# Optimization experiments

Hardware: AMD Instinct MI355X
Metric: run time of the kernel (lower is better)

## Reference

```python
import jax, jax.numpy as jnp
import numpy as np

N, D, D_A, D_B, R = 512, 4096, 256, 256, 4
B = 2048
U_END = D_B * R            # 1024
V_END = U_END + R * D_A    # 2048
B_END = V_END + D_B        # 2304
LN_EPS = 1e-5


def setup_inputs() -> dict:
    key = jax.random.key(0)
    k1, k2, k3, k4 = jax.random.split(key, 4)
    return {
        "h_A": jax.random.normal(k1, (B, D_A), dtype=jnp.float32),
        "pool_vectors": jax.random.normal(k2, (N, D), dtype=jnp.float32) * 0.02,
        "alpha": jax.random.uniform(k3, (B, N), dtype=jnp.float32),
        "W_base": jax.random.normal(k4, (D_B, D_A), dtype=jnp.float32) * 0.01,
        "b_base": jnp.zeros((D_B,), dtype=jnp.float32),
        "gamma": jnp.array(0.01, dtype=jnp.float32),
        "ln_scale": jnp.ones((D_A,), dtype=jnp.float32),
        "ln_bias": jnp.zeros((D_A,), dtype=jnp.float32),
    }


def reference(h_A, pool_vectors, alpha, W_base, b_base, gamma, ln_scale, ln_bias):
    # --- assemble ---
    U = pool_vectors[:, :U_END].reshape(N, D_B, R)          # [N, d_B, r]
    V = pool_vectors[:, U_END:V_END].reshape(N, R, D_A)     # [N, r, d_A]
    bias = pool_vectors[:, V_END:B_END]                     # [N, d_B]
    UV = jnp.einsum('ndr,nre->nde', U, V)                   # [N, d_B, d_A]
    W_assembled = W_base[None] + jnp.einsum('bn,nde->bde', alpha, UV)  # [B, d_B, d_A]
    b_assembled = b_base[None] + jnp.einsum('bn,nd->bd', alpha, bias)  # [B, d_B]
    # --- apply + residual + LayerNorm ---
    h_t = jnp.einsum('ba,bca->bc', h_A, W_assembled) + b_assembled     # [B, d_B]
    y = h_A + gamma * h_t
    mu = jnp.mean(y, axis=-1, keepdims=True)
    var = jnp.var(y, axis=-1, keepdims=True)
    y_norm = (y - mu) * jax.lax.rsqrt(var + LN_EPS)
    return y_norm * ln_scale + ln_bias
```

## Files before the change

### kernel.cpp

```cpp
#include <hip/hip_runtime.h>
#include <hip/hip_bf16.h>


typedef __attribute__((ext_vector_type(8))) short bf16x8;
typedef __attribute__((ext_vector_type(4))) float f32x4;
typedef unsigned short ushort_t;

#define LDA_X 2816
#define N_POOL 512
#define D_POOL 4096

__device__ __forceinline__ void gld16(const ushort_t* g, ushort_t* l) {
    __builtin_amdgcn_global_load_lds((__attribute__((address_space(1))) void*)g,
                                     (__attribute__((address_space(3))) void*)l, 16, 0, 0);
}

__device__ __forceinline__ ushort_t bfb(float x) {
    union { __hip_bfloat16 h; ushort_t u; } c; c.h = __float2bfloat16(x); return c.u;
}

__device__ __forceinline__ float bf2f(ushort_t u) {
    union { unsigned int i; float f; } c; c.i = ((unsigned int)u) << 16; return c.f;
}

__device__ __forceinline__ void write4(ushort_t* p, float4 v) {
    ushort4 w = {bfb(v.x), bfb(v.y), bfb(v.z), bfb(v.w)};
    *(ushort4*)p = w;
}

__global__ __launch_bounds__(256) void kFront(const float* __restrict__ hA,
                                              const float* __restrict__ pool,
                                              const float* __restrict__ alpha,
                                              const float* __restrict__ Wb,
                                              ushort_t* __restrict__ Xu,
                                              ushort_t* __restrict__ Mt,
                                              ushort_t* __restrict__ part) {
    __shared__ __align__(16) ushort_t shmem[16384];
    ushort_t* As = shmem;
    ushort_t* Bs = shmem + 8192;
    const int t = threadIdx.x;
    const int bid = blockIdx.x;

    if (bid >= 1024 && bid < 1536) {
        int idx = (bid - 1024) * 256 + t, c = idx >> 9, n = idx & 511;
        write4(Mt + (size_t)c * LDA_X + (n << 2), *(const float4*)&pool[(size_t)n * D_POOL + (c << 2)]);
        return;
    }

    const int w = t >> 6, l = t & 63, l16 = l & 15, l4 = l >> 4;
    const int wr = w >> 1, wc = w & 1;
    const int row = t >> 2, cs = t & 3;

    f32x4 acc[2][2];
    #pragma unroll
    for (int i = 0; i < 2; ++i)
        #pragma unroll
        for (int j = 0; j < 2; ++j) acc[i][j] = (f32x4){0.f, 0.f, 0.f, 0.f};

    float4 aR[4], bR[4];

    auto writeLDS_AB = [&](int buf) {
        #pragma unroll
        for (int p = 0; p < 4; ++p) {
            int c0 = (cs + p * 4) << 2;
            int off = row * 64 + (((c0 >> 3) ^ (row & 7)) << 3) + ((c0 >> 2) & 1) * 4;
            ushort4 ua = {bfb(aR[p].x), bfb(aR[p].y), bfb(aR[p].z), bfb(aR[p].w)};
            ushort4 ub = {bfb(bR[p].x), bfb(bR[p].y), bfb(bR[p].z), bfb(bR[p].w)};
            *(ushort4*)&As[buf * 4096 + off] = ua;
            *(ushort4*)&Bs[buf * 4096 + off] = ub;
        }
    };
    auto compute = [&](int buf) {
        bf16x8 af[2][2], bv[2][2];
        #pragma unroll
        for (int mi = 0; mi < 2; ++mi) {
            int arow = wr * 32 + mi * 16 + l16;
            #pragma unroll
            for (int ks = 0; ks < 2; ++ks)
                af[mi][ks] = *(const bf16x8*)&As[buf * 4096 + arow * 64 + (((ks * 4 + l4) ^ (arow & 7)) << 3)];
        }
        #pragma unroll
        for (int ni = 0; ni < 2; ++ni) {
            int brow = wc * 32 + ni * 16 + l16;
            #pragma unroll
            for (int ks = 0; ks < 2; ++ks)
                bv[ni][ks] = *(const bf16x8*)&Bs[buf * 4096 + brow * 64 + (((ks * 4 + l4) ^ (brow & 7)) << 3)];
        }
        #pragma unroll
        for (int ks = 0; ks < 2; ++ks)
            #pragma unroll
            for (int mi = 0; mi < 2; ++mi)
                #pragma unroll
                for (int ni = 0; ni < 2; ++ni)
                    acc[mi][ni] = __builtin_amdgcn_mfma_f32_16x16x32_bf16(af[mi][ks], bv[ni][ks], acc[mi][ni], 0, 0, 0);
    };
    auto epilogueLDS = [&]() {
        __syncthreads();
        float* sc = (float*)shmem;
        #pragma unroll
        for (int mi = 0; mi < 2; ++mi)
            #pragma unroll
            for (int ni = 0; ni < 2; ++ni)
                #pragma unroll
                for (int e = 0; e < 4; ++e)
                    sc[(wr * 32 + mi * 16 + l4 * 4 + e) * 64 + wc * 32 + ni * 16 + l16] = acc[mi][ni][e];
        __syncthreads();
    };

    if (bid < 1024) {
        const int bm0 = (bid >> 5) * 64, bn0 = (bid & 31) * 64;
        const int kk = bn0 + row;
        const float* bbase = pool + (size_t)(kk >> 2) * D_POOL + 1024 + (kk & 3) * 256;
        const float* abase = hA + (size_t)(bm0 + row) * 256;
        auto loadRegs = [&](int step) {
            const int a0 = step * 64;
            #pragma unroll
            for (int p = 0; p < 4; ++p) {
                int c0 = (cs + p * 4) << 2;
                aR[p] = *(const float4*)(abase + a0 + c0);
                bR[p] = *(const float4*)(bbase + a0 + c0);
            }
        };
        loadRegs(0); writeLDS_AB(0); __syncthreads();
        int cur = 0;
        #pragma unroll
        for (int it = 0; it < 3; ++it) {
            loadRegs(it + 1);
            compute(cur);
            writeLDS_AB(cur ^ 1);
            __syncthreads();
            cur ^= 1;
        }
        compute(cur);
        epilogueLDS();
        float* sc = (float*)shmem;
        const int r2 = t >> 2, c0 = (t & 3) * 16;
        const float* arow = alpha + (size_t)(bm0 + r2) * N_POOL;
        __align__(16) ushort_t u[16];
        #pragma unroll
        for (int j = 0; j < 16; ++j)
            u[j] = bfb(sc[r2 * 64 + c0 + j] * arow[(bn0 + c0 + j) >> 2]);
        ushort_t* dst = Xu + (size_t)(bm0 + r2) * LDA_X + bn0 + c0;
        *(uint4*)dst = ((uint4*)u)[0];
        *(uint4*)(dst + 8) = ((uint4*)u)[1];
        return;
    }

    if (bid < 1664) {
        const int b2 = bid - 1536;
        const int bm0 = (b2 >> 2) * 64, bc0 = (b2 & 3) * 64;
        const float* abase = hA + (size_t)(bm0 + row) * 256;
        const float* bbase = Wb + (size_t)(bc0 + row) * 256;
        auto loadRegs = [&](int step) {
            const int a0 = step * 64;
            #pragma unroll
            for (int p = 0; p < 4; ++p) {
                int c0 = (cs + p * 4) << 2;
                aR[p] = *(const float4*)(abase + a0 + c0);
                bR[p] = *(const float4*)(bbase + a0 + c0);
            }
        };
        loadRegs(0); writeLDS_AB(0); __syncthreads();
        int cur = 0;
        #pragma unroll
        for (int it = 0; it < 3; ++it) {
            loadRegs(it + 1);
            compute(cur);
            writeLDS_AB(cur ^ 1);
            __syncthreads();
            cur ^= 1;
        }
        compute(cur);
        epilogueLDS();
        float* sc = (float*)shmem;
        const int r2 = t >> 2, c0 = (t & 3) * 16;
        __align__(16) ushort_t u[16];
        #pragma unroll
        for (int j = 0; j < 16; ++j) u[j] = bfb(sc[r2 * 64 + c0 + j]);
        ushort_t* P = part + (size_t)8 * (2048 * 256) + (size_t)(bm0 + r2) * 256 + bc0 + c0;
        *(uint4*)P = ((uint4*)u)[0];
        *(uint4*)(P + 8) = ((uint4*)u)[1];
        return;
    }

    {
        const int b2 = bid - 1664;
        const int bm0 = (b2 >> 2) * 64, bc0 = (b2 & 3) * 64;
        const float* abase = alpha + (size_t)(bm0 + row) * N_POOL;
        const int cg = t & 63;
        const int jg = t >> 6;
        float bRv[16];
        auto loadRegsB = [&](int step) {
            const int j0 = step * 64;
            #pragma unroll
            for (int p = 0; p < 4; ++p) {
                int c0 = (cs + p * 4) << 2;
                aR[p] = *(const float4*)(abase + j0 + c0);
            }
            #pragma unroll
            for (int p = 0; p < 16; ++p)
                bRv[p] = pool[(size_t)(j0 + jg * 16 + p) * D_POOL + 2048 + bc0 + cg];
        };
        auto writeLDSB = [&](int buf) {
            #pragma unroll
            for (int p = 0; p < 4; ++p) {
                int c0 = (cs + p * 4) << 2;
                int off = row * 64 + (((c0 >> 3) ^ (row & 7)) << 3) + ((c0 >> 2) & 1) * 4;
                ushort4 ua = {bfb(aR[p].x), bfb(aR[p].y), bfb(aR[p].z), bfb(aR[p].w)};
                *(ushort4*)&As[buf * 4096 + off] = ua;
            }
            #pragma unroll
            for (int p = 0; p < 16; ++p) {
                int jj = jg * 16 + p;
                Bs[buf * 4096 + cg * 64 + (((jj >> 3) ^ (cg & 7)) << 3) + (jj & 7)] = bfb(bRv[p]);
            }
        };
        loadRegsB(0); writeLDSB(0); __syncthreads();
        int cur = 0;
        #pragma unroll
        for (int it = 0; it < 7; ++it) {
            loadRegsB(it + 1);
            compute(cur);
            writeLDSB(cur ^ 1);
            __syncthreads();
            cur ^= 1;
        }
        compute(cur);
        epilogueLDS();
        float* sc = (float*)shmem;
        const int r2 = t >> 2, c0 = (t & 3) * 16;
        __align__(16) ushort_t u[16];
        #pragma unroll
        for (int j = 0; j < 16; ++j) u[j] = bfb(sc[r2 * 64 + c0 + j]);
        ushort_t* P = part + (size_t)9 * (2048 * 256) + (size_t)(bm0 + r2) * 256 + bc0 + c0;
        *(uint4*)P = ((uint4*)u)[0];
        *(uint4*)(P + 8) = ((uint4*)u)[1];
    }
}

__global__ __launch_bounds__(256) void kB(const ushort_t* __restrict__ Xu,
                                          const ushort_t* __restrict__ Mt,
                                          ushort_t* __restrict__ part) {
    __shared__ __align__(16) ushort_t As[2][4096];
    __shared__ __align__(16) ushort_t Bs[2][4096];
    const int t = threadIdx.x;
    const int w = t >> 6, l = t & 63, l16 = l & 15, l4 = l >> 4;
    const int wr = w >> 1, wc = w & 1;
    const int bid = blockIdx.x;
    const int z = bid & 7;
    const int n = (bid >> 3) & 3;
    const int m = bid >> 5;
    const int bm0 = m * 64, bn0 = n * 64;
    const int kc0 = z * 256;
    const int srow = t >> 3;
    const int schunk = (t & 7) ^ (srow & 7);

    f32x4 acc[2][2];
    #pragma unroll
    for (int i = 0; i < 2; ++i)
        #pragma unroll
        for (int j = 0; j < 2; ++j) acc[i][j] = (f32x4){0.f, 0.f, 0.f, 0.f};

    auto stage = [&](int buf, int k0) {
        #pragma unroll
        for (int h = 0; h < 2; ++h) {
            gld16(Xu + (size_t)(bm0 + srow + h * 32) * LDA_X + k0 + schunk * 8,
                  &As[buf][h * 2048 + w * 512]);
            gld16(Mt + (size_t)(bn0 + srow + h * 32) * LDA_X + k0 + schunk * 8,
                  &Bs[buf][h * 2048 + w * 512]);
        }
    };
    auto compute = [&](int buf) {
        bf16x8 af[2][2], bv[2][2];
        #pragma unroll
        for (int mi = 0; mi < 2; ++mi) {
            int arow = wr * 32 + mi * 16 + l16;
            #pragma unroll
            for (int ks = 0; ks < 2; ++ks)
                af[mi][ks] = *(const bf16x8*)&As[buf][arow * 64 + (((ks * 4 + l4) ^ (arow & 7)) << 3)];
        }
        #pragma unroll
        for (int ni = 0; ni < 2; ++ni) {
            int brow = wc * 32 + ni * 16 + l16;
            #pragma unroll
            for (int ks = 0; ks < 2; ++ks)
                bv[ni][ks] = *(const bf16x8*)&Bs[buf][brow * 64 + (((ks * 4 + l4) ^ (brow & 7)) << 3)];
        }
        #pragma unroll
        for (int ks = 0; ks < 2; ++ks)
            #pragma unroll
            for (int mi = 0; mi < 2; ++mi)
                #pragma unroll
                for (int ni = 0; ni < 2; ++ni)
                    acc[mi][ni] = __builtin_amdgcn_mfma_f32_16x16x32_bf16(af[mi][ks], bv[ni][ks], acc[mi][ni], 0, 0, 0);
    };

    stage(0, kc0);
    __syncthreads();
    int cur = 0;
    #pragma unroll
    for (int it = 0; it < 3; ++it) {
        stage(cur ^ 1, kc0 + (it + 1) * 64);
        compute(cur);
        __syncthreads();
        cur ^= 1;
    }
    compute(cur);

    __syncthreads();
    float* sc = (float*)&As[0][0];
    #pragma unroll
    for (int mi = 0; mi < 2; ++mi)
        #pragma unroll
        for (int ni = 0; ni < 2; ++ni)
            #pragma unroll
            for (int e = 0; e < 4; ++e)
                sc[(wr * 32 + mi * 16 + l4 * 4 + e) * 64 + wc * 32 + ni * 16 + l16] = acc[mi][ni][e];
    __syncthreads();
    const int r2 = t >> 2, c0 = (t & 3) * 16;
    __align__(16) ushort_t u[16];
    #pragma unroll
    for (int j = 0; j < 16; ++j) u[j] = bfb(sc[r2 * 64 + c0 + j]);
    ushort_t* P = part + (size_t)z * (2048 * 256) + (size_t)(bm0 + r2) * 256 + bn0 + c0;
    *(uint4*)P = ((uint4*)u)[0];
    *(uint4*)(P + 8) = ((uint4*)u)[1];
}

__global__ __launch_bounds__(256) void kC(const ushort_t* __restrict__ part,
                                          const float* __restrict__ hA,
                                          const float* __restrict__ bb,
                                          const float* __restrict__ gamma_p,
                                          const float* __restrict__ lns,
                                          const float* __restrict__ lnb,
                                          float* __restrict__ out) {
    const int wave = threadIdx.x >> 6;
    const int lane = threadIdx.x & 63;
    const int b = blockIdx.x * 4 + wave;
    const float g = gamma_p[0];
    const size_t base = (size_t)b * 256 + lane * 4;

    float p0 = 0.f, p1 = 0.f, p2 = 0.f, p3 = 0.f;
    #pragma unroll
    for (int z = 0; z < 10; ++z) {
        ushort4 q = *(const ushort4*)&part[(size_t)z * 2048 * 256 + base];
        p0 += bf2f(q.x); p1 += bf2f(q.y); p2 += bf2f(q.z); p3 += bf2f(q.w);
    }
    float4 h  = *(const float4*)&hA[base];
    float4 b4 = *(const float4*)&bb[lane * 4];
    float y0 = h.x + g * (p0 + b4.x);
    float y1 = h.y + g * (p1 + b4.y);
    float y2 = h.z + g * (p2 + b4.z);
    float y3 = h.w + g * (p3 + b4.w);

    float sum = y0 + y1 + y2 + y3;
    float ss  = y0*y0 + y1*y1 + y2*y2 + y3*y3;
    #pragma unroll
    for (int off = 1; off < 64; off <<= 1) {
        sum += __shfl_xor(sum, off);
        ss  += __shfl_xor(ss, off);
    }
    float mu  = sum * (1.0f / 256.0f);
    float var = ss * (1.0f / 256.0f) - mu * mu;
    float inv = rsqrtf(var + 1e-5f);

    float4 sc = *(const float4*)&lns[lane * 4];
    float4 bi = *(const float4*)&lnb[lane * 4];
    float4 o;
    o.x = (y0 - mu) * inv * sc.x + bi.x;
    o.y = (y1 - mu) * inv * sc.y + bi.y;
    o.z = (y2 - mu) * inv * sc.z + bi.z;
    o.w = (y3 - mu) * inv * sc.w + bi.w;
    *(float4*)&out[base] = o;
}

extern "C" void kernel_launch(void* const* d_in, const int* in_sizes, int n_in,
                              void* d_out, int out_size, void* d_ws, size_t ws_size,
                              hipStream_t stream) {
    const float* hA    = (const float*)d_in[0];
    const float* pool  = (const float*)d_in[1];
    const float* alpha = (const float*)d_in[2];
    const float* Wb    = (const float*)d_in[3];
    const float* bb    = (const float*)d_in[4];
    const float* gamma = (const float*)d_in[5];
    const float* lns   = (const float*)d_in[6];
    const float* lnb   = (const float*)d_in[7];
    float* out = (float*)d_out;

    ushort_t* Xu   = (ushort_t*)d_ws;
    ushort_t* Mt   = Xu + (size_t)2048 * LDA_X;
    ushort_t* part = Mt + (size_t)256 * LDA_X;

    kFront<<<1792, 256, 0, stream>>>(hA, pool, alpha, Wb, Xu, Mt, part);
    kB<<<1024, 256, 0, stream>>>(Xu, Mt, part);
    kC<<<512, 256, 0, stream>>>(part, hA, bb, gamma, lns, lnb, out);
}
```

Baseline: 35.39 us.

## Fuse V-projection and U-expansion GEMMs into one kernel, keeping intermediate in LDS

Merges the front kernel's hA·V GEMM and the second-stage GEMM against U into a single kernel. Each block owns 64 batch rows and a 64-pool-vector slice, and keeps the alpha-scaled intermediate in LDS as bf16. This drops the global Xu/Mt workspaces, the transpose pass and one kernel launch. Per-block work grows (64x256 tiles, 512 blocks total), so occupancy is lower and fewer blocks are available to fill the GPU.

```diff
diff --git a/kernel.cpp b/kernel.cpp
--- a/kernel.cpp
+++ b/kernel.cpp
@@ -6,14 +6,8 @@
 typedef __attribute__((ext_vector_type(4))) float f32x4;
 typedef unsigned short ushort_t;
 
-#define LDA_X 2816
 #define N_POOL 512
 #define D_POOL 4096
-
-__device__ __forceinline__ void gld16(const ushort_t* g, ushort_t* l) {
-    __builtin_amdgcn_global_load_lds((__attribute__((address_space(1))) void*)g,
-                                     (__attribute__((address_space(3))) void*)l, 16, 0, 0);
-}
 
 __device__ __forceinline__ ushort_t bfb(float x) {
     union { __hip_bfloat16 h; ushort_t u; } c; c.h = __float2bfloat16(x); return c.u;
@@ -23,31 +17,192 @@
     union { unsigned int i; float f; } c; c.i = ((unsigned int)u) << 16; return c.f;
 }
 
-__device__ __forceinline__ void write4(ushort_t* p, float4 v) {
-    ushort4 w = {bfb(v.x), bfb(v.y), bfb(v.z), bfb(v.w)};
-    *(ushort4*)p = w;
-}
-
-__global__ __launch_bounds__(256) void kFront(const float* __restrict__ hA,
+__global__ __launch_bounds__(256) void kFused(const float* __restrict__ hA,
                                               const float* __restrict__ pool,
                                               const float* __restrict__ alpha,
                                               const float* __restrict__ Wb,
-                                              ushort_t* __restrict__ Xu,
-                                              ushort_t* __restrict__ Mt,
                                               ushort_t* __restrict__ part) {
-    __shared__ __align__(16) ushort_t shmem[16384];
-    ushort_t* As = shmem;
-    ushort_t* Bs = shmem + 8192;
+    __shared__ __align__(16) ushort_t shm[36864];
     const int t = threadIdx.x;
     const int bid = blockIdx.x;
-
-    if (bid >= 1024 && bid < 1536) {
-        int idx = (bid - 1024) * 256 + t, c = idx >> 9, n = idx & 511;
-        write4(Mt + (size_t)c * LDA_X + (n << 2), *(const float4*)&pool[(size_t)n * D_POOL + (c << 2)]);
+    const int w = t >> 6, l = t & 63, l16 = l & 15, l4 = l >> 4;
+
+    if (bid < 256) {
+        ushort_t* As = shm;
+        ushort_t* Bs = shm + 4096;
+        ushort_t* S_ = shm + 20480;
+        const int m = bid >> 3, z = bid & 7;
+        const int b0 = m * 64;
+
+        f32x4 acc[4][4];
+        #pragma unroll
+        for (int i = 0; i < 4; ++i)
+            #pragma unroll
+            for (int j = 0; j < 4; ++j) acc[i][j] = (f32x4){0.f, 0.f, 0.f, 0.f};
+
+        float4 regA[2], regB[8];
+        const int rA = t >> 2, cA = t & 3;
+
+        auto compute = [&](int buf) {
+            bf16x8 af[4], bv[4];
+            #pragma unroll
+            for (int mi = 0; mi < 4; ++mi) {
+                int ar = mi * 16 + l16;
+                af[mi] = *(const bf16x8*)&As[buf * 2048 + ar * 32 + ((l4 ^ ((ar >> 1) & 3)) << 3)];
+            }
+            #pragma unroll
+            for (int ni = 0; ni < 4; ++ni) {
+                int br = w * 64 + ni * 16 + l16;
+                bv[ni] = *(const bf16x8*)&Bs[buf * 8192 + br * 32 + ((l4 ^ ((br >> 1) & 3)) << 3)];
+            }
+            #pragma unroll
+            for (int mi = 0; mi < 4; ++mi)
+                #pragma unroll
+                for (int ni = 0; ni < 4; ++ni)
+                    acc[mi][ni] = __builtin_amdgcn_mfma_f32_16x16x32_bf16(af[mi], bv[ni], acc[mi][ni], 0, 0, 0);
+        };
+
+        const float* aBase = hA + (size_t)(b0 + rA) * 256;
+        auto loadA1 = [&](int st) {
+            regA[0] = *(const float4*)(aBase + st * 32 + cA * 8);
+            regA[1] = *(const float4*)(aBase + st * 32 + cA * 8 + 4);
+        };
+        auto loadB1 = [&](int st) {
+            #pragma unroll
+            for (int p = 0; p < 8; ++p) {
+                int n_off = w * 16 + p * 2 + (l >> 5);
+                int q = (l >> 3) & 3, a_off = (l & 7) * 4;
+                regB[p] = *(const float4*)&pool[(size_t)(z * 64 + n_off) * D_POOL + 1024 + q * 256 + st * 32 + a_off];
+            }
+        };
+        auto writeA = [&](int buf) {
+            int ch = cA ^ ((rA >> 1) & 3);
+            ushort4 u0 = {bfb(regA[0].x), bfb(regA[0].y), bfb(regA[0].z), bfb(regA[0].w)};
+            ushort4 u1 = {bfb(regA[1].x), bfb(regA[1].y), bfb(regA[1].z), bfb(regA[1].w)};
+            *(ushort4*)&As[buf * 2048 + rA * 32 + (ch << 3)] = u0;
+            *(ushort4*)&As[buf * 2048 + rA * 32 + (ch << 3) + 4] = u1;
+        };
+        auto writeB1 = [&](int buf) {
+            #pragma unroll
+            for (int p = 0; p < 8; ++p) {
+                int n_off = w * 16 + p * 2 + (l >> 5);
+                int q = (l >> 3) & 3;
+                int krel = n_off * 4 + q;
+                int chunk = (l & 7) >> 1, half = (l & 7) & 1;
+                ushort4 u = {bfb(regB[p].x), bfb(regB[p].y), bfb(regB[p].z), bfb(regB[p].w)};
+                *(ushort4*)&Bs[buf * 8192 + krel * 32 + ((chunk ^ ((krel >> 1) & 3)) << 3) + half * 4] = u;
+            }
+        };
+
+        loadA1(0); loadB1(0); writeA(0); writeB1(0);
+        __syncthreads();
+        int cur = 0;
+        #pragma unroll
+        for (int it = 0; it < 7; ++it) {
+            loadA1(it + 1); loadB1(it + 1);
+            compute(cur);
+            writeA(cur ^ 1); writeB1(cur ^ 1);
+            __syncthreads();
+            cur ^= 1;
+        }
+        compute(cur);
+
+        #pragma unroll
+        for (int mi = 0; mi < 4; ++mi)
+            #pragma unroll
+            for (int ni = 0; ni < 4; ++ni) {
+                int col = w * 64 + ni * 16 + l16;
+                #pragma unroll
+                for (int e = 0; e < 4; ++e) {
+                    int row = mi * 16 + l4 * 4 + e;
+                    float av = alpha[(size_t)(b0 + row) * N_POOL + z * 64 + (col >> 2)];
+                    int ch = (col >> 3) ^ (row & 7);
+                    S_[row * 256 + (ch << 3) + (col & 7)] = bfb(acc[mi][ni][e] * av);
+                }
+                acc[mi][ni] = (f32x4){0.f, 0.f, 0.f, 0.f};
+            }
+        __syncthreads();
+
+        auto loadB2 = [&](int st) {
+            #pragma unroll
+            for (int p = 0; p < 8; ++p) {
+                int n_off = w * 2 + (p >> 2);
+                int cblk = p & 3;
+                regB[p] = *(const float4*)&pool[(size_t)(z * 64 + st * 8 + n_off) * D_POOL + (cblk * 64 + l) * 4];
+            }
+        };
+        auto writeB2 = [&](int buf) {
+            #pragma unroll
+            for (int p = 0; p < 8; ++p) {
+                int n_off = w * 2 + (p >> 2);
+                int c = (p & 3) * 64 + l;
+                int chunk = n_off >> 1, half = n_off & 1;
+                ushort4 u = {bfb(regB[p].x), bfb(regB[p].y), bfb(regB[p].z), bfb(regB[p].w)};
+                *(ushort4*)&Bs[buf * 8192 + c * 32 + ((chunk ^ ((c >> 1) & 3)) << 3) + half * 4] = u;
+            }
+        };
+        auto compute2 = [&](int buf, int st) {
+            bf16x8 af[4], bv[4];
+            #pragma unroll
+            for (int mi = 0; mi < 4; ++mi) {
+                int ar = mi * 16 + l16;
+                int ch = (st * 4 + l4) ^ (ar & 7);
+                af[mi] = *(const bf16x8*)&S_[ar * 256 + (ch << 3)];
+            }
+            #pragma unroll
+            for (int ni = 0; ni < 4; ++ni) {
+                int br = w * 64 + ni * 16 + l16;
+                bv[ni] = *(const bf16x8*)&Bs[buf * 8192 + br * 32 + ((l4 ^ ((br >> 1) & 3)) << 3)];
+            }
+            #pragma unroll
+            for (int mi = 0; mi < 4; ++mi)
+                #pragma unroll
+                for (int ni = 0; ni < 4; ++ni)
+                    acc[mi][ni] = __builtin_amdgcn_mfma_f32_16x16x32_bf16(af[mi], bv[ni], acc[mi][ni], 0, 0, 0);
+        };
+
+        loadB2(0); writeB2(0);
+        __syncthreads();
+        cur = 0;
+        #pragma unroll
+        for (int it = 0; it < 7; ++it) {
+            loadB2(it + 1);
+            compute2(cur, it);
+            writeB2(cur ^ 1);
+            __syncthreads();
+            cur ^= 1;
+        }
+        compute2(cur, 7);
+
+        __syncthreads();
+        #pragma unroll
+        for (int mi = 0; mi < 4; ++mi)
+            #pragma unroll
+            for (int ni = 0; ni < 4; ++ni) {
+                int col = w * 64 + ni * 16 + l16;
+                #pragma unroll
+                for (int e = 0; e < 4; ++e) {
+                    int row = mi * 16 + l4 * 4 + e;
+                    int ch = (col >> 3) ^ (row & 7);
+                    S_[row * 256 + (ch << 3) + (col & 7)] = bfb(acc[mi][ni][e]);
+                }
+            }
+        __syncthreads();
+        {
+            int row = t >> 2;
+            ushort_t* P = part + (size_t)z * (2048 * 256) + (size_t)(b0 + row) * 256;
+            #pragma unroll
+            for (int p = 0; p < 8; ++p) {
+                int ch = (t & 3) * 8 + p;
+                bf16x8 v = *(const bf16x8*)&S_[row * 256 + ((ch ^ (row & 7)) << 3)];
+                *(bf16x8*)&P[ch * 8] = v;
+            }
+        }
         return;
     }
 
-    const int w = t >> 6, l = t & 63, l16 = l & 15, l4 = l >> 4;
+    ushort_t* As = shm;
+    ushort_t* Bs = shm + 8192;
     const int wr = w >> 1, wc = w & 1;
     const int row = t >> 2, cs = t & 3;
 
@@ -70,7 +225,7 @@
             *(ushort4*)&Bs[buf * 4096 + off] = ub;
         }
     };
-    auto compute = [&](int buf) {
+    auto compute64 = [&](int buf) {
         bf16x8 af[2][2], bv[2][2];
         #pragma unroll
         for (int mi = 0; mi < 2; ++mi) {
@@ -96,7 +251,7 @@
     };
     auto epilogueLDS = [&]() {
         __syncthreads();
-        float* sc = (float*)shmem;
+        float* sc = (float*)shm;
         #pragma unroll
         for (int mi = 0; mi < 2; ++mi)
             #pragma unroll
@@ -107,47 +262,8 @@
         __syncthreads();
     };
 
-    if (bid < 1024) {
-        const int bm0 = (bid >> 5) * 64, bn0 = (bid & 31) * 64;
-        const int kk = bn0 + row;
-        const float* bbase = pool + (size_t)(kk >> 2) * D_POOL + 1024 + (kk & 3) * 256;
-        const float* abase = hA + (size_t)(bm0 + row) * 256;
-        auto loadRegs = [&](int step) {
-            const int a0 = step * 64;
-            #pragma unroll
-            for (int p = 0; p < 4; ++p) {
-                int c0 = (cs + p * 4) << 2;
-                aR[p] = *(const float4*)(abase + a0 + c0);
-                bR[p] = *(const float4*)(bbase + a0 + c0);
-            }
-        };
-        loadRegs(0); writeLDS_AB(0); __syncthreads();
-        int cur = 0;
-        #pragma unroll
-        for (int it = 0; it < 3; ++it) {
-            loadRegs(it + 1);
-            compute(cur);
-            writeLDS_AB(cur ^ 1);
-            __syncthreads();
-            cur ^= 1;
-        }
-        compute(cur);
-        epilogueLDS();
-        float* sc = (float*)shmem;
-        const int r2 = t >> 2, c0 = (t & 3) * 16;
-        const float* arow = alpha + (size_t)(bm0 + r2) * N_POOL;
-        __align__(16) ushort_t u[16];
-        #pragma unroll
-        for (int j = 0; j < 16; ++j)
-            u[j] = bfb(sc[r2 * 64 + c0 + j] * arow[(bn0 + c0 + j) >> 2]);
-        ushort_t* dst = Xu + (size_t)(bm0 + r2) * LDA_X + bn0 + c0;
-        *(uint4*)dst = ((uint4*)u)[0];
-        *(uint4*)(dst + 8) = ((uint4*)u)[1];
-        return;
-    }
-
-    if (bid < 1664) {
-        const int b2 = bid - 1536;
+    if (bid < 384) {
+        const int b2 = bid - 256;
         const int bm0 = (b2 >> 2) * 64, bc0 = (b2 & 3) * 64;
         const float* abase = hA + (size_t)(bm0 + row) * 256;
         const float* bbase = Wb + (size_t)(bc0 + row) * 256;
@@ -165,14 +281,14 @@
         #pragma unroll
         for (int it = 0; it < 3; ++it) {
             loadRegs(it + 1);
-            compute(cur);
+            compute64(cur);
             writeLDS_AB(cur ^ 1);
             __syncthreads();
             cur ^= 1;
         }
-        compute(cur);
+        compute64(cur);
         epilogueLDS();
-        float* sc = (float*)shmem;
+        float* sc = (float*)shm;
         const int r2 = t >> 2, c0 = (t & 3) * 16;
         __align__(16) ushort_t u[16];
         #pragma unroll
@@ -184,7 +300,7 @@
     }
 
     {
-        const int b2 = bid - 1664;
+        const int b2 = bid - 384;
         const int bm0 = (b2 >> 2) * 64, bc0 = (b2 & 3) * 64;
         const float* abase = alpha + (size_t)(bm0 + row) * N_POOL;
         const int cg = t & 63;
@@ -220,14 +336,14 @@
         #pragma unroll
         for (int it = 0; it < 7; ++it) {
             loadRegsB(it + 1);
-            compute(cur);
+            compute64(cur);
             writeLDSB(cur ^ 1);
             __syncthreads();
             cur ^= 1;
         }
-        compute(cur);
+        compute64(cur);
         epilogueLDS();
-        float* sc = (float*)shmem;
+        float* sc = (float*)shm;
         const int r2 = t >> 2, c0 = (t & 3) * 16;
         __align__(16) ushort_t u[16];
         #pragma unroll
@@ -236,94 +352,6 @@
         *(uint4*)P = ((uint4*)u)[0];
         *(uint4*)(P + 8) = ((uint4*)u)[1];
     }
-}
-
-__global__ __launch_bounds__(256) void kB(const ushort_t* __restrict__ Xu,
-                                          const ushort_t* __restrict__ Mt,
-                                          ushort_t* __restrict__ part) {
-    __shared__ __align__(16) ushort_t As[2][4096];
-    __shared__ __align__(16) ushort_t Bs[2][4096];
-    const int t = threadIdx.x;
-    const int w = t >> 6, l = t & 63, l16 = l & 15, l4 = l >> 4;
-    const int wr = w >> 1, wc = w & 1;
-    const int bid = blockIdx.x;
-    const int z = bid & 7;
-    const int n = (bid >> 3) & 3;
-    const int m = bid >> 5;
-    const int bm0 = m * 64, bn0 = n * 64;
-    const int kc0 = z * 256;
-    const int srow = t >> 3;
-    const int schunk = (t & 7) ^ (srow & 7);
-
-    f32x4 acc[2][2];
-    #pragma unroll
-    for (int i = 0; i < 2; ++i)
-        #pragma unroll
-        for (int j = 0; j < 2; ++j) acc[i][j] = (f32x4){0.f, 0.f, 0.f, 0.f};
-
-    auto stage = [&](int buf, int k0) {
-        #pragma unroll
-        for (int h = 0; h < 2; ++h) {
-            gld16(Xu + (size_t)(bm0 + srow + h * 32) * LDA_X + k0 + schunk * 8,
-                  &As[buf][h * 2048 + w * 512]);
-            gld16(Mt + (size_t)(bn0 + srow + h * 32) * LDA_X + k0 + schunk * 8,
-                  &Bs[buf][h * 2048 + w * 512]);
-        }
-    };
-    auto compute = [&](int buf) {
-        bf16x8 af[2][2], bv[2][2];
-        #pragma unroll
-        for (int mi = 0; mi < 2; ++mi) {
-            int arow = wr * 32 + mi * 16 + l16;
-            #pragma unroll
-            for (int ks = 0; ks < 2; ++ks)
-                af[mi][ks] = *(const bf16x8*)&As[buf][arow * 64 + (((ks * 4 + l4) ^ (arow & 7)) << 3)];
-        }
-        #pragma unroll
-        for (int ni = 0; ni < 2; ++ni) {
-            int brow = wc * 32 + ni * 16 + l16;
-            #pragma unroll
-            for (int ks = 0; ks < 2; ++ks)
-                bv[ni][ks] = *(const bf16x8*)&Bs[buf][brow * 64 + (((ks * 4 + l4) ^ (brow & 7)) << 3)];
-        }
-        #pragma unroll
-        for (int ks = 0; ks < 2; ++ks)
-            #pragma unroll
-            for (int mi = 0; mi < 2; ++mi)
-                #pragma unroll
-                for (int ni = 0; ni < 2; ++ni)
-                    acc[mi][ni] = __builtin_amdgcn_mfma_f32_16x16x32_bf16(af[mi][ks], bv[ni][ks], acc[mi][ni], 0, 0, 0);
-    };
-
-    stage(0, kc0);
-    __syncthreads();
-    int cur = 0;
-    #pragma unroll
-    for (int it = 0; it < 3; ++it) {
-        stage(cur ^ 1, kc0 + (it + 1) * 64);
-        compute(cur);
-        __syncthreads();
-        cur ^= 1;
-    }
-    compute(cur);
-
-    __syncthreads();
-    float* sc = (float*)&As[0][0];
-    #pragma unroll
-    for (int mi = 0; mi < 2; ++mi)
-        #pragma unroll
-        for (int ni = 0; ni < 2; ++ni)
-            #pragma unroll
-            for (int e = 0; e < 4; ++e)
-                sc[(wr * 32 + mi * 16 + l4 * 4 + e) * 64 + wc * 32 + ni * 16 + l16] = acc[mi][ni][e];
-    __syncthreads();
-    const int r2 = t >> 2, c0 = (t & 3) * 16;
-    __align__(16) ushort_t u[16];
-    #pragma unroll
-    for (int j = 0; j < 16; ++j) u[j] = bfb(sc[r2 * 64 + c0 + j]);
-    ushort_t* P = part + (size_t)z * (2048 * 256) + (size_t)(bm0 + r2) * 256 + bn0 + c0;
-    *(uint4*)P = ((uint4*)u)[0];
-    *(uint4*)(P + 8) = ((uint4*)u)[1];
 }
 
 __global__ __launch_bounds__(256) void kC(const ushort_t* __restrict__ part,
@@ -386,11 +414,8 @@
     const float* lnb   = (const float*)d_in[7];
     float* out = (float*)d_out;
 
-    ushort_t* Xu   = (ushort_t*)d_ws;
-    ushort_t* Mt   = Xu + (size_t)2048 * LDA_X;
-    ushort_t* part = Mt + (size_t)256 * LDA_X;
-
-    kFront<<<1792, 256, 0, stream>>>(hA, pool, alpha, Wb, Xu, Mt, part);
-    kB<<<1024, 256, 0, stream>>>(Xu, Mt, part);
+    ushort_t* part = (ushort_t*)d_ws;
+
+    kFused<<<512, 256, 0, stream>>>(hA, pool, alpha, Wb, part);
     kC<<<512, 256, 0, stream>>>(part, hA, bb, gamma, lns, lnb, out);
 }
```

Measured after the change: 31.66 us. 1.12x faster.
